# Performance work log

Hardware: AMD Instinct MI355X
Metric: run time of the kernel (lower is better)

## Reference

```python
import jax, jax.numpy as jnp
import numpy as np

B = 131072          # batch size
D = 128             # input_dim
OUT = 64            # output_dim
L = 32              # number of masked (CustomizedLinear) layers = hidden + output nodes


def setup_inputs() -> dict:
    key = jax.random.key(0)
    ks = jax.random.split(key, 8)
    x = jax.random.normal(ks[0], (B, D), dtype=jnp.float32)
    # start_node: nn.Linear(D, D)
    w_start = jax.random.normal(ks[1], (D, D), dtype=jnp.float32) / np.sqrt(D)
    b_start = jnp.zeros((D,), dtype=jnp.float32)
    # masked linear layers: weight elementwise-multiplied by binary graph mask
    raw_w = jax.random.normal(ks[2], (L, D, D), dtype=jnp.float32) / np.sqrt(D)
    mask = (jax.random.uniform(ks[3], (L, D, D)) < 0.25).astype(jnp.float32)
    masked_w = raw_w * mask          # [L, D, D]
    layer_b = jnp.zeros((L, D), dtype=jnp.float32)
    # output_layer: nn.Linear(D, OUT)
    w_out = jax.random.normal(ks[4], (OUT, D), dtype=jnp.float32) / np.sqrt(D)
    b_out = jnp.zeros((OUT,), dtype=jnp.float32)
    return {"x": x, "w_start": w_start, "b_start": b_start,
            "masked_w": masked_w, "layer_b": layer_b,
            "w_out": w_out, "b_out": b_out}


def reference(x, w_start, b_start, masked_w, layer_b, w_out, b_out):
    # x = start_node(x)
    x0 = x @ w_start.T + b_start          # [B, D]

    # sequential masked-linear chain with relu + residual back to x0
    def step(h, params):
        w, b = params                      # w: [D, D], b: [D]
        h = jax.nn.relu(h @ w.T + b) + x0  # x_ = relu(layer(x_)) + x
        return h, None

    h, _ = jax.lax.scan(step, x0, (masked_w, layer_b))

    logits = h @ w_out.T + b_out          # [B, OUT]
    return jax.nn.softmax(logits, axis=1)
```

## Files before the change

kernel.cpp:

```cpp
#include <hip/hip_runtime.h>
#include <hip/hip_bf16.h>
#include <stdint.h>


typedef short bs8 __attribute__((ext_vector_type(8)));
typedef float f32x4 __attribute__((ext_vector_type(4)));

union Frag {
  bs8 v;
  uint32_t u[4];
};

__device__ __forceinline__ uint16_t f2bf_rne(float f) {
  union { float f; uint32_t u; } c; c.f = f;
  uint32_t r = c.u + 0x7fffu + ((c.u >> 16) & 1u);
  return (uint16_t)(r >> 16);
}

__device__ __forceinline__ uint32_t pack2bf(float lo, float hi) {
  float2 t; t.x = lo; t.y = hi;
  __hip_bfloat162 b = __float22bfloat162_rn(t);
  union { __hip_bfloat162 b; uint32_t u; } c; c.b = b;
  return c.u;
}

__global__ void prep_frags(const float* __restrict__ w_start,
                           const float* __restrict__ masked_w,
                           const float* __restrict__ w_out,
                           uint16_t* __restrict__ dst) {
  int e = blockIdx.x * 256 + threadIdx.x;
  if (e >= 548864) return;
  int j    = e & 7;
  int lane = (e >> 3) & 63;
  int kt   = (e >> 9) & 3;
  int q    = lane >> 4;
  int m15  = lane & 15;
  float val;
  if (e < 16384) {
    int nt = (e >> 11) & 7;
    int n = nt * 16 + m15;
    int k = q * 8 + j + kt * 32;
    val = w_start[n * 128 + k];
  } else if (e < 540672) {
    int e2 = e - 16384;
    int l  = e2 >> 14;
    int nt = (e2 >> 11) & 7;
    int n = nt * 16 + m15;
    int k = q * 4 + (j & 3) + 16 * (j >> 2) + kt * 32;
    val = masked_w[(l * 128 + n) * 128 + k];
  } else {
    int e2 = e - 540672;
    int nt = (e2 >> 11) & 3;
    int n = nt * 16 + m15;
    int k = q * 4 + (j & 3) + 16 * (j >> 2) + kt * 32;
    val = w_out[n * 128 + k];
  }
  dst[e] = f2bf_rne(val);
}

extern __shared__ uint16_t lds[];

__global__ void __launch_bounds__(256, 2)
wann_main(const float* __restrict__ x,
          const float* __restrict__ b_start,
          const float* __restrict__ layer_b,
          const float* __restrict__ b_out,
          const uint16_t* __restrict__ wfrag,
          float* __restrict__ out) {
  const int tid  = threadIdx.x;
  const int lane = tid & 63;
  const int wave = tid >> 6;
  const int q    = lane >> 4;
  const int mc   = lane & 15;
  const long batch0 = (long)blockIdx.x * 256 + wave * 64;

  uint16_t* bufA = lds;
  uint16_t* bufB = lds + 16384;

  auto stage_buf = [&](uint16_t* dstb, const uint16_t* srcb) {
    #pragma unroll
    for (int i = 0; i < 8; ++i) {
      __builtin_amdgcn_global_load_lds(
          (const __attribute__((address_space(1))) void*)(srcb + i * 2048 + wave * 512 + lane * 8),
          (__attribute__((address_space(3))) void*)(dstb + i * 2048 + wave * 512),
          16, 0, 0);
    }
  };

  stage_buf(bufA, wfrag);

  Frag xf[4][4];
  #pragma unroll
  for (int mt = 0; mt < 4; ++mt) {
    const float* xrow = x + (batch0 + mt * 16 + mc) * 128 + q * 8;
    #pragma unroll
    for (int kt = 0; kt < 4; ++kt) {
      float4 a = *reinterpret_cast<const float4*>(xrow + kt * 32);
      float4 b = *reinterpret_cast<const float4*>(xrow + kt * 32 + 4);
      xf[mt][kt].u[0] = pack2bf(a.x, a.y);
      xf[mt][kt].u[1] = pack2bf(a.z, a.w);
      xf[mt][kt].u[2] = pack2bf(b.x, b.y);
      xf[mt][kt].u[3] = pack2bf(b.z, b.w);
    }
  }

  __syncthreads();
  stage_buf(bufB, wfrag + 16384);

  Frag x0f[4][4];
  Frag hfr[4][4];
  #pragma unroll
  for (int p = 0; p < 4; ++p) {
    f32x4 acc[2][4];
    #pragma unroll
    for (int ntl = 0; ntl < 2; ++ntl) {
      const int nt = 2 * p + ntl;
      const float4 bb = *reinterpret_cast<const float4*>(b_start + nt * 16 + q * 4);
      #pragma unroll
      for (int mt = 0; mt < 4; ++mt) {
        acc[ntl][mt][0] = bb.x; acc[ntl][mt][1] = bb.y;
        acc[ntl][mt][2] = bb.z; acc[ntl][mt][3] = bb.w;
      }
    }
    #pragma unroll
    for (int kt = 0; kt < 4; ++kt) {
      #pragma unroll
      for (int ntl = 0; ntl < 2; ++ntl) {
        const int nt = 2 * p + ntl;
        Frag wf;
        wf.v = *reinterpret_cast<const bs8*>(bufA + ((nt * 4 + kt) * 64 + lane) * 8);
        #pragma unroll
        for (int mt = 0; mt < 4; ++mt)
          acc[ntl][mt] = __builtin_amdgcn_mfma_f32_16x16x32_bf16(wf.v, xf[mt][kt].v, acc[ntl][mt], 0, 0, 0);
      }
    }
    #pragma unroll
    for (int mt = 0; mt < 4; ++mt) {
      #pragma unroll
      for (int ntl = 0; ntl < 2; ++ntl) {
        x0f[mt][p].u[2 * ntl + 0] = pack2bf(acc[ntl][mt][0], acc[ntl][mt][1]);
        x0f[mt][p].u[2 * ntl + 1] = pack2bf(acc[ntl][mt][2], acc[ntl][mt][3]);
      }
    }
  }
  #pragma unroll
  for (int mt = 0; mt < 4; ++mt)
    #pragma unroll
    for (int kt = 0; kt < 4; ++kt)
      hfr[mt][kt].v = x0f[mt][kt].v;

  const uint16_t* chain = wfrag + 16384;
  for (int l = 0; l < 32; ++l) {
    __syncthreads();
    uint16_t* wl  = (l & 1) ? bufA : bufB;
    uint16_t* nxt = (l & 1) ? bufB : bufA;
    if (l < 31) stage_buf(nxt, chain + (l + 1) * 16384);
    const float* bl = layer_b + l * 128;

    uint32_t tq[3][4][4];
    #pragma unroll
    for (int p = 0; p < 4; ++p) {
      f32x4 acc[2][4];
      #pragma unroll
      for (int ntl = 0; ntl < 2; ++ntl) {
        const int nt = 2 * p + ntl;
        const float4 bb = *reinterpret_cast<const float4*>(bl + nt * 16 + q * 4);
        #pragma unroll
        for (int mt = 0; mt < 4; ++mt) {
          acc[ntl][mt][0] = bb.x; acc[ntl][mt][1] = bb.y;
          acc[ntl][mt][2] = bb.z; acc[ntl][mt][3] = bb.w;
        }
      }
      #pragma unroll
      for (int kt = 0; kt < 4; ++kt) {
        #pragma unroll
        for (int ntl = 0; ntl < 2; ++ntl) {
          const int nt = 2 * p + ntl;
          Frag wf;
          wf.v = *reinterpret_cast<const bs8*>(wl + ((nt * 4 + kt) * 64 + lane) * 8);
          #pragma unroll
          for (int mt = 0; mt < 4; ++mt)
            acc[ntl][mt] = __builtin_amdgcn_mfma_f32_16x16x32_bf16(wf.v, hfr[mt][kt].v, acc[ntl][mt], 0, 0, 0);
        }
      }
      #pragma unroll
      for (int mt = 0; mt < 4; ++mt) {
        #pragma unroll
        for (int ntl = 0; ntl < 2; ++ntl) {
          uint32_t xw0 = x0f[mt][p].u[2 * ntl + 0];
          uint32_t xw1 = x0f[mt][p].u[2 * ntl + 1];
          float v0 = fmaxf(acc[ntl][mt][0], 0.0f) + __uint_as_float(xw0 << 16);
          float v1 = fmaxf(acc[ntl][mt][1], 0.0f) + __uint_as_float(xw0 & 0xffff0000u);
          float v2 = fmaxf(acc[ntl][mt][2], 0.0f) + __uint_as_float(xw1 << 16);
          float v3 = fmaxf(acc[ntl][mt][3], 0.0f) + __uint_as_float(xw1 & 0xffff0000u);
          uint32_t pw0 = pack2bf(v0, v1);
          uint32_t pw1 = pack2bf(v2, v3);
          if (p < 3) {
            tq[p][mt][2 * ntl + 0] = pw0;
            tq[p][mt][2 * ntl + 1] = pw1;
          } else {
            hfr[mt][3].u[2 * ntl + 0] = pw0;
            hfr[mt][3].u[2 * ntl + 1] = pw1;
          }
        }
      }
    }
    #pragma unroll
    for (int mt = 0; mt < 4; ++mt)
      #pragma unroll
      for (int p = 0; p < 3; ++p)
        #pragma unroll
        for (int w = 0; w < 4; ++w)
          hfr[mt][p].u[w] = tq[p][mt][w];
  }

  const uint16_t* wout = wfrag + 540672;
  f32x4 ao[4][4];
  #pragma unroll
  for (int nt = 0; nt < 4; ++nt) {
    const float4 bb = *reinterpret_cast<const float4*>(b_out + nt * 16 + q * 4);
    #pragma unroll
    for (int mt = 0; mt < 4; ++mt) {
      ao[nt][mt][0] = bb.x; ao[nt][mt][1] = bb.y;
      ao[nt][mt][2] = bb.z; ao[nt][mt][3] = bb.w;
    }
  }
  #pragma unroll
  for (int kt = 0; kt < 4; ++kt) {
    #pragma unroll
    for (int nt = 0; nt < 4; ++nt) {
      Frag wf;
      wf.v = *reinterpret_cast<const bs8*>(wout + ((nt * 4 + kt) * 64 + lane) * 8);
      #pragma unroll
      for (int mt = 0; mt < 4; ++mt)
        ao[nt][mt] = __builtin_amdgcn_mfma_f32_16x16x32_bf16(wf.v, hfr[mt][kt].v, ao[nt][mt], 0, 0, 0);
    }
  }

  float* tr = reinterpret_cast<float*>(lds + 16384) + wave * 1088;
  #pragma unroll
  for (int mt = 0; mt < 4; ++mt) {
    float e[16];
    float M = -3.0e38f;
    #pragma unroll
    for (int nt = 0; nt < 4; ++nt)
      #pragma unroll
      for (int r = 0; r < 4; ++r)
        M = fmaxf(M, ao[nt][mt][r]);
    M = fmaxf(M, __shfl_xor(M, 16, 64));
    M = fmaxf(M, __shfl_xor(M, 32, 64));
    float S = 0.0f;
    #pragma unroll
    for (int nt = 0; nt < 4; ++nt)
      #pragma unroll
      for (int r = 0; r < 4; ++r) {
        float t = exp2f((ao[nt][mt][r] - M) * 1.4426950408889634f);
        e[nt * 4 + r] = t;
        S += t;
      }
    S += __shfl_xor(S, 16, 64);
    S += __shfl_xor(S, 32, 64);
    const float inv = 1.0f / S;
    #pragma unroll
    for (int nt = 0; nt < 4; ++nt) {
      float4 pv;
      pv.x = e[nt * 4 + 0] * inv;
      pv.y = e[nt * 4 + 1] * inv;
      pv.z = e[nt * 4 + 2] * inv;
      pv.w = e[nt * 4 + 3] * inv;
      *reinterpret_cast<float4*>(tr + mc * 68 + nt * 16 + q * 4) = pv;
    }
    __asm__ volatile("s_waitcnt lgkmcnt(0)" ::: "memory");
    #pragma unroll
    for (int it = 0; it < 4; ++it) {
      int row = it * 4 + (lane >> 4);
      float4 v = *reinterpret_cast<const float4*>(tr + row * 68 + (lane & 15) * 4);
      long gr = batch0 + mt * 16 + row;
      *reinterpret_cast<float4*>(out + gr * 64 + (lane & 15) * 4) = v;
    }
    __asm__ volatile("s_waitcnt lgkmcnt(0)" ::: "memory");
  }
}

extern "C" void kernel_launch(void* const* d_in, const int* in_sizes, int n_in,
                              void* d_out, int out_size, void* d_ws, size_t ws_size,
                              hipStream_t stream) {
  const float* x        = (const float*)d_in[0];
  const float* w_start  = (const float*)d_in[1];
  const float* b_start  = (const float*)d_in[2];
  const float* masked_w = (const float*)d_in[3];
  const float* layer_b  = (const float*)d_in[4];
  const float* w_out    = (const float*)d_in[5];
  const float* b_out    = (const float*)d_in[6];
  uint16_t* wfrag = (uint16_t*)d_ws;

  prep_frags<<<2144, 256, 0, stream>>>(w_start, masked_w, w_out, wfrag);
  wann_main<<<512, 256, 65536, stream>>>(x, b_start, layer_b, b_out, wfrag,
                                         (float*)d_out);
}
```

Before: 294.6 us.

## Ping-pong hidden-state fragments, use hardware bf16 packing, vectorize weight prep

The chain loop is restructured to alternate between two register fragment sets (hA/hB), unrolled by two, which removes the temporary tq copy and the per-layer register shuffling. Bias is fed directly as the MFMA accumulator input on the first k-step rather than being broadcast beforehand. Float-to-bf16 conversion uses the packed hardware conversion builtin when it is available. The prep kernel now has each thread produce eight values and do one 16-byte store. More fragment arrays may raise register pressure at the two-waves-per-SIMD launch bound.

```diff
diff --git a/kernel.cpp b/kernel.cpp
--- a/kernel.cpp
+++ b/kernel.cpp
@@ -6,56 +6,50 @@
 typedef short bs8 __attribute__((ext_vector_type(8)));
 typedef float f32x4 __attribute__((ext_vector_type(4)));
 
-union Frag {
-  bs8 v;
-  uint32_t u[4];
-};
-
-__device__ __forceinline__ uint16_t f2bf_rne(float f) {
-  union { float f; uint32_t u; } c; c.f = f;
-  uint32_t r = c.u + 0x7fffu + ((c.u >> 16) & 1u);
-  return (uint16_t)(r >> 16);
-}
-
-__device__ __forceinline__ uint32_t pack2bf(float lo, float hi) {
-  float2 t; t.x = lo; t.y = hi;
-  __hip_bfloat162 b = __float22bfloat162_rn(t);
-  union { __hip_bfloat162 b; uint32_t u; } c; c.b = b;
-  return c.u;
+union Frag { bs8 v; uint32_t u[4]; };
+union F4   { float4 f; f32x4 v; };
+
+__device__ __forceinline__ uint32_t cvtpk(float lo, float hi) {
+#if __has_builtin(__builtin_amdgcn_cvt_pk_bf16_f32)
+  auto r = __builtin_amdgcn_cvt_pk_bf16_f32(lo, hi);
+  uint32_t u; __builtin_memcpy(&u, &r, 4);
+  return u;
+#else
+  union { float f; uint32_t u; } a, b; a.f = lo; b.f = hi;
+  uint32_t ra = a.u + 0x7fffu + ((a.u >> 16) & 1u);
+  uint32_t rb = b.u + 0x7fffu + ((b.u >> 16) & 1u);
+  return (ra >> 16) | (rb & 0xffff0000u);
+#endif
 }
 
 __global__ void prep_frags(const float* __restrict__ w_start,
                            const float* __restrict__ masked_w,
                            const float* __restrict__ w_out,
                            uint16_t* __restrict__ dst) {
-  int e = blockIdx.x * 256 + threadIdx.x;
-  if (e >= 548864) return;
-  int j    = e & 7;
-  int lane = (e >> 3) & 63;
-  int kt   = (e >> 9) & 3;
-  int q    = lane >> 4;
-  int m15  = lane & 15;
-  float val;
-  if (e < 16384) {
-    int nt = (e >> 11) & 7;
-    int n = nt * 16 + m15;
-    int k = q * 8 + j + kt * 32;
-    val = w_start[n * 128 + k];
-  } else if (e < 540672) {
-    int e2 = e - 16384;
-    int l  = e2 >> 14;
-    int nt = (e2 >> 11) & 7;
-    int n = nt * 16 + m15;
-    int k = q * 4 + (j & 3) + 16 * (j >> 2) + kt * 32;
-    val = masked_w[(l * 128 + n) * 128 + k];
+  int t = blockIdx.x * 256 + threadIdx.x;
+  if (t >= 68608) return;
+  int lane = t & 63, kt = (t >> 6) & 3, q = lane >> 4, m15 = lane & 15;
+  float f[8];
+  if (t < 2048) {
+    int nt = (t >> 8) & 7;
+    const float* s = w_start + (nt * 16 + m15) * 128 + q * 8 + kt * 32;
+    #pragma unroll
+    for (int j = 0; j < 8; ++j) f[j] = s[j];
+  } else if (t < 67584) {
+    int t2 = t - 2048, l = t2 >> 11, nt = (t2 >> 8) & 7;
+    const float* s = masked_w + ((l * 128) + nt * 16 + m15) * 128 + q * 4 + kt * 32;
+    #pragma unroll
+    for (int j = 0; j < 8; ++j) f[j] = s[(j & 3) + 16 * (j >> 2)];
   } else {
-    int e2 = e - 540672;
-    int nt = (e2 >> 11) & 3;
-    int n = nt * 16 + m15;
-    int k = q * 4 + (j & 3) + 16 * (j >> 2) + kt * 32;
-    val = w_out[n * 128 + k];
-  }
-  dst[e] = f2bf_rne(val);
+    int t3 = t - 67584, nt = (t3 >> 8) & 3;
+    const float* s = w_out + (nt * 16 + m15) * 128 + q * 4 + kt * 32;
+    #pragma unroll
+    for (int j = 0; j < 8; ++j) f[j] = s[(j & 3) + 16 * (j >> 2)];
+  }
+  uint4 o;
+  o.x = cvtpk(f[0], f[1]); o.y = cvtpk(f[2], f[3]);
+  o.z = cvtpk(f[4], f[5]); o.w = cvtpk(f[6], f[7]);
+  *reinterpret_cast<uint4*>(dst + t * 8) = o;
 }
 
 extern __shared__ uint16_t lds[];
@@ -73,6 +67,7 @@
   const int q    = lane >> 4;
   const int mc   = lane & 15;
   const long batch0 = (long)blockIdx.x * 256 + wave * 64;
+  const f32x4 zero4 = {0.f, 0.f, 0.f, 0.f};
 
   uint16_t* bufA = lds;
   uint16_t* bufB = lds + 16384;
@@ -97,31 +92,23 @@
     for (int kt = 0; kt < 4; ++kt) {
       float4 a = *reinterpret_cast<const float4*>(xrow + kt * 32);
       float4 b = *reinterpret_cast<const float4*>(xrow + kt * 32 + 4);
-      xf[mt][kt].u[0] = pack2bf(a.x, a.y);
-      xf[mt][kt].u[1] = pack2bf(a.z, a.w);
-      xf[mt][kt].u[2] = pack2bf(b.x, b.y);
-      xf[mt][kt].u[3] = pack2bf(b.z, b.w);
+      xf[mt][kt].u[0] = cvtpk(a.x, a.y);
+      xf[mt][kt].u[1] = cvtpk(a.z, a.w);
+      xf[mt][kt].u[2] = cvtpk(b.x, b.y);
+      xf[mt][kt].u[3] = cvtpk(b.z, b.w);
     }
   }
 
   __syncthreads();
   stage_buf(bufB, wfrag + 16384);
 
-  Frag x0f[4][4];
-  Frag hfr[4][4];
+  Frag x0f[4][4], hA[4][4], hB[4][4];
   #pragma unroll
   for (int p = 0; p < 4; ++p) {
+    F4 bb[2];
+    bb[0].f = *reinterpret_cast<const float4*>(b_start + (2 * p + 0) * 16 + q * 4);
+    bb[1].f = *reinterpret_cast<const float4*>(b_start + (2 * p + 1) * 16 + q * 4);
     f32x4 acc[2][4];
-    #pragma unroll
-    for (int ntl = 0; ntl < 2; ++ntl) {
-      const int nt = 2 * p + ntl;
-      const float4 bb = *reinterpret_cast<const float4*>(b_start + nt * 16 + q * 4);
-      #pragma unroll
-      for (int mt = 0; mt < 4; ++mt) {
-        acc[ntl][mt][0] = bb.x; acc[ntl][mt][1] = bb.y;
-        acc[ntl][mt][2] = bb.z; acc[ntl][mt][3] = bb.w;
-      }
-    }
     #pragma unroll
     for (int kt = 0; kt < 4; ++kt) {
       #pragma unroll
@@ -130,47 +117,29 @@
         Frag wf;
         wf.v = *reinterpret_cast<const bs8*>(bufA + ((nt * 4 + kt) * 64 + lane) * 8);
         #pragma unroll
-        for (int mt = 0; mt < 4; ++mt)
-          acc[ntl][mt] = __builtin_amdgcn_mfma_f32_16x16x32_bf16(wf.v, xf[mt][kt].v, acc[ntl][mt], 0, 0, 0);
-      }
-    }
-    #pragma unroll
-    for (int mt = 0; mt < 4; ++mt) {
+        for (int mt = 0; mt < 4; ++mt) {
+          f32x4 c = (kt == 0) ? bb[ntl].v : acc[ntl][mt];
+          acc[ntl][mt] = __builtin_amdgcn_mfma_f32_16x16x32_bf16(wf.v, xf[mt][kt].v, c, 0, 0, 0);
+        }
+      }
+    }
+    #pragma unroll
+    for (int mt = 0; mt < 4; ++mt)
       #pragma unroll
       for (int ntl = 0; ntl < 2; ++ntl) {
-        x0f[mt][p].u[2 * ntl + 0] = pack2bf(acc[ntl][mt][0], acc[ntl][mt][1]);
-        x0f[mt][p].u[2 * ntl + 1] = pack2bf(acc[ntl][mt][2], acc[ntl][mt][3]);
-      }
-    }
-  }
-  #pragma unroll
-  for (int mt = 0; mt < 4; ++mt)
-    #pragma unroll
-    for (int kt = 0; kt < 4; ++kt)
-      hfr[mt][kt].v = x0f[mt][kt].v;
-
-  const uint16_t* chain = wfrag + 16384;
-  for (int l = 0; l < 32; ++l) {
-    __syncthreads();
-    uint16_t* wl  = (l & 1) ? bufA : bufB;
-    uint16_t* nxt = (l & 1) ? bufB : bufA;
-    if (l < 31) stage_buf(nxt, chain + (l + 1) * 16384);
-    const float* bl = layer_b + l * 128;
-
-    uint32_t tq[3][4][4];
+        x0f[mt][p].u[2 * ntl + 0] = cvtpk(acc[ntl][mt][0], acc[ntl][mt][1]);
+        x0f[mt][p].u[2 * ntl + 1] = cvtpk(acc[ntl][mt][2], acc[ntl][mt][3]);
+      }
+  }
+
+  auto chain_layer = [&](const uint16_t* wl, const float* bl,
+                         Frag (&hin)[4][4], Frag (&hout)[4][4]) {
     #pragma unroll
     for (int p = 0; p < 4; ++p) {
+      F4 bb[2];
+      bb[0].f = *reinterpret_cast<const float4*>(bl + (2 * p + 0) * 16 + q * 4);
+      bb[1].f = *reinterpret_cast<const float4*>(bl + (2 * p + 1) * 16 + q * 4);
       f32x4 acc[2][4];
-      #pragma unroll
-      for (int ntl = 0; ntl < 2; ++ntl) {
-        const int nt = 2 * p + ntl;
-        const float4 bb = *reinterpret_cast<const float4*>(bl + nt * 16 + q * 4);
-        #pragma unroll
-        for (int mt = 0; mt < 4; ++mt) {
-          acc[ntl][mt][0] = bb.x; acc[ntl][mt][1] = bb.y;
-          acc[ntl][mt][2] = bb.z; acc[ntl][mt][3] = bb.w;
-        }
-      }
       #pragma unroll
       for (int kt = 0; kt < 4; ++kt) {
         #pragma unroll
@@ -179,52 +148,54 @@
           Frag wf;
           wf.v = *reinterpret_cast<const bs8*>(wl + ((nt * 4 + kt) * 64 + lane) * 8);
           #pragma unroll
-          for (int mt = 0; mt < 4; ++mt)
-            acc[ntl][mt] = __builtin_amdgcn_mfma_f32_16x16x32_bf16(wf.v, hfr[mt][kt].v, acc[ntl][mt], 0, 0, 0);
+          for (int mt = 0; mt < 4; ++mt) {
+            f32x4 c = (kt == 0) ? bb[ntl].v : acc[ntl][mt];
+            acc[ntl][mt] = __builtin_amdgcn_mfma_f32_16x16x32_bf16(wf.v, hin[mt][kt].v, c, 0, 0, 0);
+          }
         }
       }
       #pragma unroll
       for (int mt = 0; mt < 4; ++mt) {
         #pragma unroll
         for (int ntl = 0; ntl < 2; ++ntl) {
+          f32x4 r = __builtin_elementwise_max(acc[ntl][mt], zero4);
           uint32_t xw0 = x0f[mt][p].u[2 * ntl + 0];
           uint32_t xw1 = x0f[mt][p].u[2 * ntl + 1];
-          float v0 = fmaxf(acc[ntl][mt][0], 0.0f) + __uint_as_float(xw0 << 16);
-          float v1 = fmaxf(acc[ntl][mt][1], 0.0f) + __uint_as_float(xw0 & 0xffff0000u);
-          float v2 = fmaxf(acc[ntl][mt][2], 0.0f) + __uint_as_float(xw1 << 16);
-          float v3 = fmaxf(acc[ntl][mt][3], 0.0f) + __uint_as_float(xw1 & 0xffff0000u);
-          uint32_t pw0 = pack2bf(v0, v1);
-          uint32_t pw1 = pack2bf(v2, v3);
-          if (p < 3) {
-            tq[p][mt][2 * ntl + 0] = pw0;
-            tq[p][mt][2 * ntl + 1] = pw1;
-          } else {
-            hfr[mt][3].u[2 * ntl + 0] = pw0;
-            hfr[mt][3].u[2 * ntl + 1] = pw1;
-          }
+          f32x4 xv;
+          xv[0] = __uint_as_float(xw0 << 16);
+          xv[1] = __uint_as_float(xw0 & 0xffff0000u);
+          xv[2] = __uint_as_float(xw1 << 16);
+          xv[3] = __uint_as_float(xw1 & 0xffff0000u);
+          r = r + xv;
+          hout[mt][p].u[2 * ntl + 0] = cvtpk(r[0], r[1]);
+          hout[mt][p].u[2 * ntl + 1] = cvtpk(r[2], r[3]);
         }
       }
     }
-    #pragma unroll
-    for (int mt = 0; mt < 4; ++mt)
-      #pragma unroll
-      for (int p = 0; p < 3; ++p)
-        #pragma unroll
-        for (int w = 0; w < 4; ++w)
-          hfr[mt][p].u[w] = tq[p][mt][w];
-  }
+  };
+
+  const uint16_t* chain = wfrag + 16384;
+  __syncthreads();
+  stage_buf(bufA, chain + 16384);
+  chain_layer(bufB, layer_b, x0f, hB);
+  #pragma unroll 1
+  for (int l = 1; l < 31; l += 2) {
+    __syncthreads();
+    stage_buf(bufB, chain + (l + 1) * 16384);
+    chain_layer(bufA, layer_b + l * 128, hB, hA);
+    __syncthreads();
+    if (l + 2 < 32) stage_buf(bufA, chain + (l + 2) * 16384);
+    chain_layer(bufB, layer_b + (l + 1) * 128, hA, hB);
+  }
+  __syncthreads();
+  chain_layer(bufA, layer_b + 31 * 128, hB, hA);
 
   const uint16_t* wout = wfrag + 540672;
+  F4 bo[4];
+  #pragma unroll
+  for (int nt = 0; nt < 4; ++nt)
+    bo[nt].f = *reinterpret_cast<const float4*>(b_out + nt * 16 + q * 4);
   f32x4 ao[4][4];
-  #pragma unroll
-  for (int nt = 0; nt < 4; ++nt) {
-    const float4 bb = *reinterpret_cast<const float4*>(b_out + nt * 16 + q * 4);
-    #pragma unroll
-    for (int mt = 0; mt < 4; ++mt) {
-      ao[nt][mt][0] = bb.x; ao[nt][mt][1] = bb.y;
-      ao[nt][mt][2] = bb.z; ao[nt][mt][3] = bb.w;
-    }
-  }
   #pragma unroll
   for (int kt = 0; kt < 4; ++kt) {
     #pragma unroll
@@ -232,8 +203,10 @@
       Frag wf;
       wf.v = *reinterpret_cast<const bs8*>(wout + ((nt * 4 + kt) * 64 + lane) * 8);
       #pragma unroll
-      for (int mt = 0; mt < 4; ++mt)
-        ao[nt][mt] = __builtin_amdgcn_mfma_f32_16x16x32_bf16(wf.v, hfr[mt][kt].v, ao[nt][mt], 0, 0, 0);
+      for (int mt = 0; mt < 4; ++mt) {
+        f32x4 c = (kt == 0) ? bo[nt].v : ao[nt][mt];
+        ao[nt][mt] = __builtin_amdgcn_mfma_f32_16x16x32_bf16(wf.v, hA[mt][kt].v, c, 0, 0, 0);
+      }
     }
   }
 
@@ -294,7 +267,7 @@
   const float* b_out    = (const float*)d_in[6];
   uint16_t* wfrag = (uint16_t*)d_ws;
 
-  prep_frags<<<2144, 256, 0, stream>>>(w_start, masked_w, w_out, wfrag);
+  prep_frags<<<268, 256, 0, stream>>>(w_start, masked_w, w_out, wfrag);
   wann_main<<<512, 256, 65536, stream>>>(x, b_start, layer_b, b_out, wfrag,
                                          (float*)d_out);
 }
```

After: 360.8 us. 22.5% more time.
